# Kernel optimization log

Measured on AMD Instinct MI355X. Metric: run time of the kernel, lower is better.

The kernel has to match this reference:

```python
import jax, jax.numpy as jnp
import numpy as np


def setup_inputs() -> dict:
    key = jax.random.key(0)
    k1, k2 = jax.random.split(key)
    B, C, T = 32, 64, 8192
    y_pred = jax.random.normal(k1, (B, C, T), dtype=jnp.float32)
    y_true = jax.random.normal(k2, (B, C, T), dtype=jnp.float32)
    return {"y_pred": y_pred, "y_true": y_true}


def reference(y_pred, y_true):
    # Faithful to the torch code: the triu mask multiply + sum over the second
    # time axis is exactly abs_diff[b,c,t] weighted by row-sum of triu = (T - t).
    # channel_sums then sums over t and c; final reduction is a mean over batch.
    B, C, T = y_pred.shape
    abs_diff = jnp.abs(y_pred - y_true)                      # (B, C, T)
    w = jnp.arange(T, 0, -1, dtype=abs_diff.dtype)           # weight[t] = T - t
    per_batch = jnp.einsum('bct,t->b', abs_diff, w)          # (B,)
    scaling = 2.0 / (T * C * (T + 1))                        # apply_scaling_factor=True
    return scaling * jnp.mean(per_batch)
```

## Files before the change

kernel.cpp:

```cpp
#include <hip/hip_runtime.h>


#define T_DIM 8192
#define T_MASK 8191
#define BATCH 8

__global__ __launch_bounds__(256)
void wl_partial_kernel(const float4* __restrict__ a,
                       const float4* __restrict__ b,
                       float* __restrict__ partial,
                       int n4) {
    int tid = blockIdx.x * blockDim.x + threadIdx.x;
    int stride = gridDim.x * blockDim.x;

    float acc = 0.0f;
    int v = tid;

    for (; v + (BATCH - 1) * stride < n4; v += BATCH * stride) {
        float4 xa[BATCH], xb[BATCH];
        #pragma unroll
        for (int i = 0; i < BATCH; ++i) xa[i] = a[v + i * stride];
        #pragma unroll
        for (int i = 0; i < BATCH; ++i) xb[i] = b[v + i * stride];
        #pragma unroll
        for (int i = 0; i < BATCH; ++i) {
            int idx = v + i * stride;
            float w = (float)(T_DIM - ((idx << 2) & T_MASK));
            float d0 = fabsf(xa[i].x - xb[i].x);
            float d1 = fabsf(xa[i].y - xb[i].y);
            float d2 = fabsf(xa[i].z - xb[i].z);
            float d3 = fabsf(xa[i].w - xb[i].w);
            acc += w * (d0 + d1 + d2 + d3) - (d1 + 2.0f * d2 + 3.0f * d3);
        }
    }
    for (; v < n4; v += stride) {
        float4 x = a[v];
        float4 y = b[v];
        float w = (float)(T_DIM - ((v << 2) & T_MASK));
        float d0 = fabsf(x.x - y.x);
        float d1 = fabsf(x.y - y.y);
        float d2 = fabsf(x.z - y.z);
        float d3 = fabsf(x.w - y.w);
        acc += w * (d0 + d1 + d2 + d3) - (d1 + 2.0f * d2 + 3.0f * d3);
    }

    #pragma unroll
    for (int off = 32; off > 0; off >>= 1)
        acc += __shfl_down(acc, off, 64);

    __shared__ float wave_sums[4];
    int lane = threadIdx.x & 63;
    int wave = threadIdx.x >> 6;
    if (lane == 0) wave_sums[wave] = acc;
    __syncthreads();

    if (threadIdx.x == 0)
        partial[blockIdx.x] = wave_sums[0] + wave_sums[1] + wave_sums[2] + wave_sums[3];
}

__global__ __launch_bounds__(256)
void wl_final_kernel(const float* __restrict__ partial, int n,
                     float* __restrict__ out, float scale) {
    float acc = 0.0f;
    for (int i = threadIdx.x; i < n; i += 256)
        acc += partial[i];

    #pragma unroll
    for (int off = 32; off > 0; off >>= 1)
        acc += __shfl_down(acc, off, 64);

    __shared__ float wave_sums[4];
    int lane = threadIdx.x & 63;
    int wave = threadIdx.x >> 6;
    if (lane == 0) wave_sums[wave] = acc;
    __syncthreads();

    if (threadIdx.x == 0)
        out[0] = (wave_sums[0] + wave_sums[1] + wave_sums[2] + wave_sums[3]) * scale;
}

extern "C" void kernel_launch(void* const* d_in, const int* in_sizes, int n_in,
                              void* d_out, int out_size, void* d_ws, size_t ws_size,
                              hipStream_t stream) {
    const float* a = (const float*)d_in[0];
    const float* b = (const float*)d_in[1];
    float* out = (float*)d_out;
    float* partial = (float*)d_ws;

    int n = in_sizes[0];
    int n4 = n >> 2;

    const long long T = T_DIM;
    const long long C = 64;
    const long long B = (long long)n / (C * T);
    float scale = (float)(2.0 / ((double)T * (double)C * (double)(T + 1) * (double)B));

    const int threads = 256;
    const int blocks = 2048;
    wl_partial_kernel<<<blocks, threads, 0, stream>>>(
        (const float4*)a, (const float4*)b, partial, n4);
    wl_final_kernel<<<1, threads, 0, stream>>>(partial, blocks, out, scale);
}
```

Before: 146.1 us.

## Use nontemporal vector loads, split accumulators, smaller batch, more blocks

Switches the global loads to nontemporal vector loads so the streamed-once inputs are not meant to pollute caches. Interleaves the loads of the two inputs, halves the per-thread unroll batch, and doubles the grid to 4096 blocks. Uses four independent accumulators to break the serial add dependency. The smaller batch keeps fewer loads in flight per thread, which the larger grid is meant to make up for, and the final reduction now has twice as many partials to sum.

```diff
diff --git a/kernel.cpp b/kernel.cpp
--- a/kernel.cpp
+++ b/kernel.cpp
@@ -3,25 +3,28 @@
 
 #define T_DIM 8192
 #define T_MASK 8191
-#define BATCH 8
+#define BATCH 4
+
+typedef float vfloat4 __attribute__((ext_vector_type(4)));
 
 __global__ __launch_bounds__(256)
-void wl_partial_kernel(const float4* __restrict__ a,
-                       const float4* __restrict__ b,
+void wl_partial_kernel(const vfloat4* __restrict__ a,
+                       const vfloat4* __restrict__ b,
                        float* __restrict__ partial,
                        int n4) {
     int tid = blockIdx.x * blockDim.x + threadIdx.x;
     int stride = gridDim.x * blockDim.x;
 
-    float acc = 0.0f;
+    float acc0 = 0.0f, acc1 = 0.0f, acc2 = 0.0f, acc3 = 0.0f;
     int v = tid;
 
     for (; v + (BATCH - 1) * stride < n4; v += BATCH * stride) {
-        float4 xa[BATCH], xb[BATCH];
+        vfloat4 xa[BATCH], xb[BATCH];
         #pragma unroll
-        for (int i = 0; i < BATCH; ++i) xa[i] = a[v + i * stride];
-        #pragma unroll
-        for (int i = 0; i < BATCH; ++i) xb[i] = b[v + i * stride];
+        for (int i = 0; i < BATCH; ++i) {
+            xa[i] = __builtin_nontemporal_load(&a[v + i * stride]);
+            xb[i] = __builtin_nontemporal_load(&b[v + i * stride]);
+        }
         #pragma unroll
         for (int i = 0; i < BATCH; ++i) {
             int idx = v + i * stride;
@@ -30,19 +33,25 @@
             float d1 = fabsf(xa[i].y - xb[i].y);
             float d2 = fabsf(xa[i].z - xb[i].z);
             float d3 = fabsf(xa[i].w - xb[i].w);
-            acc += w * (d0 + d1 + d2 + d3) - (d1 + 2.0f * d2 + 3.0f * d3);
+            float s = w * (d0 + d1 + d2 + d3) - (d1 + 2.0f * d2 + 3.0f * d3);
+            if (i == 0) acc0 += s;
+            else if (i == 1) acc1 += s;
+            else if (i == 2) acc2 += s;
+            else acc3 += s;
         }
     }
     for (; v < n4; v += stride) {
-        float4 x = a[v];
-        float4 y = b[v];
+        vfloat4 x = __builtin_nontemporal_load(&a[v]);
+        vfloat4 y = __builtin_nontemporal_load(&b[v]);
         float w = (float)(T_DIM - ((v << 2) & T_MASK));
         float d0 = fabsf(x.x - y.x);
         float d1 = fabsf(x.y - y.y);
         float d2 = fabsf(x.z - y.z);
         float d3 = fabsf(x.w - y.w);
-        acc += w * (d0 + d1 + d2 + d3) - (d1 + 2.0f * d2 + 3.0f * d3);
+        acc0 += w * (d0 + d1 + d2 + d3) - (d1 + 2.0f * d2 + 3.0f * d3);
     }
+
+    float acc = (acc0 + acc1) + (acc2 + acc3);
 
     #pragma unroll
     for (int off = 32; off > 0; off >>= 1)
@@ -96,8 +105,8 @@
     float scale = (float)(2.0 / ((double)T * (double)C * (double)(T + 1) * (double)B));
 
     const int threads = 256;
-    const int blocks = 2048;
+    const int blocks = 4096;
     wl_partial_kernel<<<blocks, threads, 0, stream>>>(
-        (const float4*)a, (const float4*)b, partial, n4);
+        (const vfloat4*)a, (const vfloat4*)b, partial, n4);
     wl_final_kernel<<<1, threads, 0, stream>>>(partial, blocks, out, scale);
 }
```

Result: no change. 143.3 us (-1.9%).

## Stage inputs through LDS with direct global-to-LDS loads per block chunk

Applied to the files above, without the earlier changes.

Replaces the grid-stride float4 register loads with direct global_load_lds transfers of 4096-float chunks into shared memory, then reads them back as float4 from LDS. The grid changes from a fixed 2048 blocks to one block per 16384 floats, giving 1024 blocks for these inputs. The goal is to cut VGPR use and issue overhead for a bandwidth-bound reduction. In exchange it adds two barriers per chunk with no double buffering, so the loads and the compute are serialized, and the code assumes the input size is a multiple of the block size.

```diff
diff --git a/kernel.cpp b/kernel.cpp
--- a/kernel.cpp
+++ b/kernel.cpp
@@ -1,47 +1,61 @@
 #include <hip/hip_runtime.h>
+#include <stdint.h>
 
 
-#define T_DIM 8192
 #define T_MASK 8191
-#define BATCH 8
+#define T_DIMF 8192.0f
+
+#define FLOATS_PER_BLOCK 16384
+#define CHUNK_FLOATS 4096
+#define NITER (FLOATS_PER_BLOCK / CHUNK_FLOATS)
+
+__device__ __forceinline__ void load_lds16(const float* g, float* l) {
+    __builtin_amdgcn_global_load_lds(
+        (const __attribute__((address_space(1))) void*)g,
+        (__attribute__((address_space(3))) void*)l,
+        16 , 0 , 0 );
+}
 
 __global__ __launch_bounds__(256)
-void wl_partial_kernel(const float4* __restrict__ a,
-                       const float4* __restrict__ b,
-                       float* __restrict__ partial,
-                       int n4) {
-    int tid = blockIdx.x * blockDim.x + threadIdx.x;
-    int stride = gridDim.x * blockDim.x;
+void wl_partial_kernel(const float* __restrict__ a,
+                       const float* __restrict__ b,
+                       float* __restrict__ partial) {
+    __shared__ float ldsA[CHUNK_FLOATS];
+    __shared__ float ldsB[CHUNK_FLOATS];
+
+    const int tid  = threadIdx.x;
+    const int lane = tid & 63;
+    const int wave = tid >> 6;
+    const int blockBase = blockIdx.x * FLOATS_PER_BLOCK;
 
     float acc = 0.0f;
-    int v = tid;
 
-    for (; v + (BATCH - 1) * stride < n4; v += BATCH * stride) {
-        float4 xa[BATCH], xb[BATCH];
+    for (int it = 0; it < NITER; ++it) {
+        const int chunkBase = blockBase + it * CHUNK_FLOATS;
+
         #pragma unroll
-        for (int i = 0; i < BATCH; ++i) xa[i] = a[v + i * stride];
+        for (int s = 0; s < 4; ++s) {
+            const int seg = wave * 1024 + s * 256;
+            const int g   = chunkBase + seg + lane * 4;
+            load_lds16(a + g, &ldsA[seg]);
+            load_lds16(b + g, &ldsB[seg]);
+        }
+        __syncthreads();
+
         #pragma unroll
-        for (int i = 0; i < BATCH; ++i) xb[i] = b[v + i * stride];
-        #pragma unroll
-        for (int i = 0; i < BATCH; ++i) {
-            int idx = v + i * stride;
-            float w = (float)(T_DIM - ((idx << 2) & T_MASK));
-            float d0 = fabsf(xa[i].x - xb[i].x);
-            float d1 = fabsf(xa[i].y - xb[i].y);
-            float d2 = fabsf(xa[i].z - xb[i].z);
-            float d3 = fabsf(xa[i].w - xb[i].w);
+        for (int k = 0; k < 4; ++k) {
+            const int f4 = tid + k * 256;
+            float4 x = ((const float4*)ldsA)[f4];
+            float4 y = ((const float4*)ldsB)[f4];
+            const int g = chunkBase + f4 * 4;
+            float w = T_DIMF - (float)(g & T_MASK);
+            float d0 = fabsf(x.x - y.x);
+            float d1 = fabsf(x.y - y.y);
+            float d2 = fabsf(x.z - y.z);
+            float d3 = fabsf(x.w - y.w);
             acc += w * (d0 + d1 + d2 + d3) - (d1 + 2.0f * d2 + 3.0f * d3);
         }
-    }
-    for (; v < n4; v += stride) {
-        float4 x = a[v];
-        float4 y = b[v];
-        float w = (float)(T_DIM - ((v << 2) & T_MASK));
-        float d0 = fabsf(x.x - y.x);
-        float d1 = fabsf(x.y - y.y);
-        float d2 = fabsf(x.z - y.z);
-        float d3 = fabsf(x.w - y.w);
-        acc += w * (d0 + d1 + d2 + d3) - (d1 + 2.0f * d2 + 3.0f * d3);
+        __syncthreads();
     }
 
     #pragma unroll
@@ -49,12 +63,10 @@
         acc += __shfl_down(acc, off, 64);
 
     __shared__ float wave_sums[4];
-    int lane = threadIdx.x & 63;
-    int wave = threadIdx.x >> 6;
     if (lane == 0) wave_sums[wave] = acc;
     __syncthreads();
 
-    if (threadIdx.x == 0)
+    if (tid == 0)
         partial[blockIdx.x] = wave_sums[0] + wave_sums[1] + wave_sums[2] + wave_sums[3];
 }
 
@@ -88,16 +100,13 @@
     float* partial = (float*)d_ws;
 
     int n = in_sizes[0];
-    int n4 = n >> 2;
+    int blocks = n / FLOATS_PER_BLOCK;
 
-    const long long T = T_DIM;
+    const long long T = 8192;
     const long long C = 64;
     const long long B = (long long)n / (C * T);
     float scale = (float)(2.0 / ((double)T * (double)C * (double)(T + 1) * (double)B));
 
-    const int threads = 256;
-    const int blocks = 2048;
-    wl_partial_kernel<<<blocks, threads, 0, stream>>>(
-        (const float4*)a, (const float4*)b, partial, n4);
-    wl_final_kernel<<<1, threads, 0, stream>>>(partial, blocks, out, scale);
+    wl_partial_kernel<<<blocks, 256, 0, stream>>>(a, b, partial);
+    wl_final_kernel<<<1, 256, 0, stream>>>(partial, blocks, out, scale);
 }
```

Result: no change. 144.8 us (-0.9%).

## Switch to scalar nontemporal loads, four accumulators, and larger grid

Applied to the files above, without the earlier changes.

Replaces float4 vector loads with scalar float loads that use nontemporal hints. Each element's weight is now computed directly, and partial sums are spread across four independent accumulators. The grid grows from 2048 to 8192 blocks so that each load instruction stays coalesced across the wave. The aim is better streaming bandwidth and shorter dependency chains, but scalar loads issue four times as many memory instructions and the final reduction reads four times as many partial sums.

```diff
diff --git a/kernel.cpp b/kernel.cpp
--- a/kernel.cpp
+++ b/kernel.cpp
@@ -1,48 +1,47 @@
 #include <hip/hip_runtime.h>
 
 
-#define T_DIM 8192
 #define T_MASK 8191
+#define T_DIMF 8192.0f
 #define BATCH 8
 
 __global__ __launch_bounds__(256)
-void wl_partial_kernel(const float4* __restrict__ a,
-                       const float4* __restrict__ b,
+void wl_partial_kernel(const float* __restrict__ a,
+                       const float* __restrict__ b,
                        float* __restrict__ partial,
-                       int n4) {
-    int tid = blockIdx.x * blockDim.x + threadIdx.x;
-    int stride = gridDim.x * blockDim.x;
+                       int n) {
+    const int tid = blockIdx.x * blockDim.x + threadIdx.x;
+    const int stride = gridDim.x * blockDim.x;
 
-    float acc = 0.0f;
+    float acc0 = 0.0f, acc1 = 0.0f, acc2 = 0.0f, acc3 = 0.0f;
     int v = tid;
 
-    for (; v + (BATCH - 1) * stride < n4; v += BATCH * stride) {
-        float4 xa[BATCH], xb[BATCH];
+    for (; v + (BATCH - 1) * stride < n; v += BATCH * stride) {
+        float xa[BATCH], xb[BATCH];
         #pragma unroll
-        for (int i = 0; i < BATCH; ++i) xa[i] = a[v + i * stride];
+        for (int i = 0; i < BATCH; ++i)
+            xa[i] = __builtin_nontemporal_load(&a[v + i * stride]);
         #pragma unroll
-        for (int i = 0; i < BATCH; ++i) xb[i] = b[v + i * stride];
+        for (int i = 0; i < BATCH; ++i)
+            xb[i] = __builtin_nontemporal_load(&b[v + i * stride]);
         #pragma unroll
         for (int i = 0; i < BATCH; ++i) {
-            int idx = v + i * stride;
-            float w = (float)(T_DIM - ((idx << 2) & T_MASK));
-            float d0 = fabsf(xa[i].x - xb[i].x);
-            float d1 = fabsf(xa[i].y - xb[i].y);
-            float d2 = fabsf(xa[i].z - xb[i].z);
-            float d3 = fabsf(xa[i].w - xb[i].w);
-            acc += w * (d0 + d1 + d2 + d3) - (d1 + 2.0f * d2 + 3.0f * d3);
+            int e = v + i * stride;
+            float w = T_DIMF - (float)(e & T_MASK);
+            float s = w * fabsf(xa[i] - xb[i]);
+            if ((i & 3) == 0) acc0 += s;
+            else if ((i & 3) == 1) acc1 += s;
+            else if ((i & 3) == 2) acc2 += s;
+            else acc3 += s;
         }
     }
-    for (; v < n4; v += stride) {
-        float4 x = a[v];
-        float4 y = b[v];
-        float w = (float)(T_DIM - ((v << 2) & T_MASK));
-        float d0 = fabsf(x.x - y.x);
-        float d1 = fabsf(x.y - y.y);
-        float d2 = fabsf(x.z - y.z);
-        float d3 = fabsf(x.w - y.w);
-        acc += w * (d0 + d1 + d2 + d3) - (d1 + 2.0f * d2 + 3.0f * d3);
+    for (; v < n; v += stride) {
+        float w = T_DIMF - (float)(v & T_MASK);
+        acc0 += w * fabsf(__builtin_nontemporal_load(&a[v]) -
+                          __builtin_nontemporal_load(&b[v]));
     }
+
+    float acc = (acc0 + acc1) + (acc2 + acc3);
 
     #pragma unroll
     for (int off = 32; off > 0; off >>= 1)
@@ -88,16 +87,14 @@
     float* partial = (float*)d_ws;
 
     int n = in_sizes[0];
-    int n4 = n >> 2;
 
-    const long long T = T_DIM;
+    const long long T = 8192;
     const long long C = 64;
     const long long B = (long long)n / (C * T);
     float scale = (float)(2.0 / ((double)T * (double)C * (double)(T + 1) * (double)B));
 
     const int threads = 256;
-    const int blocks = 2048;
-    wl_partial_kernel<<<blocks, threads, 0, stream>>>(
-        (const float4*)a, (const float4*)b, partial, n4);
+    const int blocks = 8192;
+    wl_partial_kernel<<<blocks, threads, 0, stream>>>(a, b, partial, n);
     wl_final_kernel<<<1, threads, 0, stream>>>(partial, blocks, out, scale);
 }
```

New measurement: 148.3 us. About the same (+1.5%).
